# Kernel tuning notes

Measured on AMD Instinct MI355X. Metric: run time of the kernel, lower is better.

## Reference

```python
import jax, jax.numpy as jnp
import numpy as np

N = 100000
E = 3200000
H = 128
C = 40


def setup_inputs() -> dict:
    key = jax.random.key(0)
    ks = jax.random.split(key, 7)
    x = jax.random.normal(ks[0], (N, H), dtype=jnp.float32)
    edge_src = jax.random.randint(ks[1], (E,), 0, N, dtype=jnp.int32)
    edge_dst = jnp.sort(jax.random.randint(ks[2], (E,), 0, N, dtype=jnp.int32))
    edge_w = jax.random.uniform(ks[3], (E,), dtype=jnp.float32)
    s = 1.0 / np.sqrt(H)
    W0 = jax.random.normal(ks[4], (H, H), dtype=jnp.float32) * s
    W1 = jax.random.normal(ks[5], (H, H), dtype=jnp.float32) * s
    W2 = jax.random.normal(ks[6], (H, C), dtype=jnp.float32) * s
    return {"x": x, "edge_src": edge_src, "edge_dst": edge_dst,
            "edge_w": edge_w, "W0": W0, "W1": W1, "W2": W2}


def _spmm(h, edge_src, edge_dst, edge_w):
    # out[i] = sum_{e: dst_e == i} w_e * h[src_e]   (sparse adj @ h)
    msgs = h[edge_src] * edge_w[:, None]          # [E, d]
    return jax.ops.segment_sum(msgs, edge_dst, num_segments=N)


def reference(x, edge_src, edge_dst, edge_w, W0, W1, W2):
    # layer 1: tanh(Linear(spmm(adj, x)))  (dropout is identity in eval mode)
    h = jnp.tanh(_spmm(x, edge_src, edge_dst, edge_w) @ W0)
    # layer 2
    h = jnp.tanh(_spmm(h, edge_src, edge_dst, edge_w) @ W1)
    # output layer (GraphConvSparse default activation is tanh here too)
    out = jnp.tanh(_spmm(h, edge_src, edge_dst, edge_w) @ W2)
    return out
```

## Files before the change

kernel.cpp:

```cpp
#include <hip/hip_runtime.h>
#include <hip/hip_fp16.h>

#define NN 100000
#define NPAD 100096
#define EE 3200000
#define HH 128
#define CC 40

typedef _Float16 f16x8 __attribute__((ext_vector_type(8)));
typedef float f32x4 __attribute__((ext_vector_type(4)));

__global__ void build_rp(const int* __restrict__ dst, int* __restrict__ rp) {
    int i = blockIdx.x * blockDim.x + threadIdx.x;
    if (i > NN) return;
    int lo = 0, hi = EE;
    while (lo < hi) {
        int mid = (lo + hi) >> 1;
        if (dst[mid] < i) lo = mid + 1; else hi = mid;
    }
    rp[i] = lo;
}

__global__ __launch_bounds__(256) void f32_to_f16(const float* __restrict__ in,
                                                  __half* __restrict__ out, int n) {
    int base = (blockIdx.x * 256 + threadIdx.x) * 8;
    if (base >= n) return;
    float4 a = *(const float4*)(in + base);
    float4 b = *(const float4*)(in + base + 4);
    __half2 h[4];
    h[0] = __floats2half2_rn(a.x, a.y);
    h[1] = __floats2half2_rn(a.z, a.w);
    h[2] = __floats2half2_rn(b.x, b.y);
    h[3] = __floats2half2_rn(b.z, b.w);
    *(float4*)(out + base) = *(float4*)h;
}

__global__ __launch_bounds__(256) void prep_edges(const int* __restrict__ src,
                                                  const float* __restrict__ w,
                                                  int4* __restrict__ ew) {
    int i = blockIdx.x * 256 + threadIdx.x;
    if (i >= EE / 4) return;
    int4 s = ((const int4*)src)[i];
    float4 f = ((const float4*)w)[i];
    int4 a, b;
    a.x = s.x; a.y = __float_as_int(f.x); a.z = s.y; a.w = __float_as_int(f.y);
    b.x = s.z; b.y = __float_as_int(f.z); b.z = s.w; b.w = __float_as_int(f.w);
    ew[2 * i] = a; ew[2 * i + 1] = b;
}

__global__ __launch_bounds__(256) void prep_weights(const float* __restrict__ W0,
                                                    const float* __restrict__ W1,
                                                    const float* __restrict__ W2,
                                                    __half* __restrict__ W0t,
                                                    __half* __restrict__ W1t,
                                                    __half* __restrict__ W2t) {
    int i = blockIdx.x * 256 + threadIdx.x;
    if (i < HH * HH) {
        int c = i >> 7, k = i & 127;
        W0t[i] = __float2half_rn(W0[k * HH + c]);
        W1t[i] = __float2half_rn(W1[k * HH + c]);
    }
    if (i < 64 * HH) {
        int c = i >> 7, k = i & 127;
        W2t[i] = __float2half_rn(c < CC ? W2[k * CC + c] : 0.f);
    }
}

__global__ __launch_bounds__(256) void spmm_h16(const __half* __restrict__ h,
                                                const int2* __restrict__ ew,
                                                const int* __restrict__ rp,
                                                __half* __restrict__ out) {
    int node = blockIdx.x * 4 + (threadIdx.x >> 6);
    int l = threadIdx.x & 63;
    if (node >= NN) return;
    int e0 = __builtin_amdgcn_readfirstlane(rp[node]);
    int e1 = __builtin_amdgcn_readfirstlane(rp[node + 1]);
    int g = l >> 4, r = l & 15;
    const f16x8* __restrict__ hrow = (const f16x8*)h;
    float acc[8] = {};
    int e = e0;
    if ((e & 1) && e < e1) {
        int2 pr = ew[e];
        float wk = (g == 0) ? __int_as_float(pr.y) : 0.f;
        f16x8 v = hrow[(size_t)pr.x * 16 + r];
#pragma unroll
        for (int j = 0; j < 8; ++j) acc[j] = fmaf(wk, (float)v[j], acc[j]);
        ++e;
    }
    int efull = e + ((e1 - e) & ~15);
    for (; e < efull; e += 16) {
        const int4* pp = (const int4*)(ew + e + 4 * g);
        int4 pa = pp[0];
        int4 pb = pp[1];
        f16x8 v0 = hrow[(size_t)pa.x * 16 + r];
        f16x8 v1 = hrow[(size_t)pa.z * 16 + r];
        f16x8 v2 = hrow[(size_t)pb.x * 16 + r];
        f16x8 v3 = hrow[(size_t)pb.z * 16 + r];
        float w0 = __int_as_float(pa.y), w1 = __int_as_float(pa.w);
        float w2 = __int_as_float(pb.y), w3 = __int_as_float(pb.w);
#pragma unroll
        for (int j = 0; j < 8; ++j) acc[j] = fmaf(w0, (float)v0[j], acc[j]);
#pragma unroll
        for (int j = 0; j < 8; ++j) acc[j] = fmaf(w1, (float)v1[j], acc[j]);
#pragma unroll
        for (int j = 0; j < 8; ++j) acc[j] = fmaf(w2, (float)v2[j], acc[j]);
#pragma unroll
        for (int j = 0; j < 8; ++j) acc[j] = fmaf(w3, (float)v3[j], acc[j]);
    }
    if (e < e1) {
#pragma unroll
        for (int k = 0; k < 4; ++k) {
            int idx = e + 4 * g + k;
            bool val = idx < e1;
            int2 pr = ew[val ? idx : e0];
            float wk = val ? __int_as_float(pr.y) : 0.f;
            f16x8 v = hrow[(size_t)pr.x * 16 + r];
#pragma unroll
            for (int j = 0; j < 8; ++j) acc[j] = fmaf(wk, (float)v[j], acc[j]);
        }
    }
#pragma unroll
    for (int j = 0; j < 8; ++j) {
        acc[j] += __shfl_xor(acc[j], 16);
        acc[j] += __shfl_xor(acc[j], 32);
    }
    if (l < 16) {
        __half2 hv[4];
#pragma unroll
        for (int j = 0; j < 4; ++j) hv[j] = __floats2half2_rn(acc[2 * j], acc[2 * j + 1]);
        *(float4*)(out + (size_t)node * HH + r * 8) = *(float4*)hv;
    }
}

__global__ __launch_bounds__(256) void spmm40_tanh(const __half* __restrict__ gpad,
                                                   const int2* __restrict__ ew,
                                                   const int* __restrict__ rp,
                                                   float* __restrict__ out) {
    int node = blockIdx.x * 4 + (threadIdx.x >> 6);
    int l = threadIdx.x & 63;
    if (node >= NN) return;
    int e0 = __builtin_amdgcn_readfirstlane(rp[node]);
    int e1 = __builtin_amdgcn_readfirstlane(rp[node + 1]);
    int g = l >> 3, r = l & 7;
    const f16x8* __restrict__ grow = (const f16x8*)gpad;
    float acc[8] = {};
    int e = e0;
    if ((e & 1) && e < e1) {
        int2 pr = ew[e];
        float wk = (g == 0) ? __int_as_float(pr.y) : 0.f;
        f16x8 v = grow[(size_t)pr.x * 8 + r];
#pragma unroll
        for (int j = 0; j < 8; ++j) acc[j] = fmaf(wk, (float)v[j], acc[j]);
        ++e;
    }
    int efull = e + ((e1 - e) & ~15);
    for (; e < efull; e += 16) {
        int4 pa = *(const int4*)(ew + e + 2 * g);
        f16x8 v0 = grow[(size_t)pa.x * 8 + r];
        f16x8 v1 = grow[(size_t)pa.z * 8 + r];
        float w0 = __int_as_float(pa.y), w1 = __int_as_float(pa.w);
#pragma unroll
        for (int j = 0; j < 8; ++j) acc[j] = fmaf(w0, (float)v0[j], acc[j]);
#pragma unroll
        for (int j = 0; j < 8; ++j) acc[j] = fmaf(w1, (float)v1[j], acc[j]);
    }
    if (e < e1) {
#pragma unroll
        for (int k = 0; k < 2; ++k) {
            int idx = e + 2 * g + k;
            bool val = idx < e1;
            int2 pr = ew[val ? idx : e0];
            float wk = val ? __int_as_float(pr.y) : 0.f;
            f16x8 v = grow[(size_t)pr.x * 8 + r];
#pragma unroll
            for (int j = 0; j < 8; ++j) acc[j] = fmaf(wk, (float)v[j], acc[j]);
        }
    }
#pragma unroll
    for (int j = 0; j < 8; ++j) {
        acc[j] += __shfl_xor(acc[j], 8);
        acc[j] += __shfl_xor(acc[j], 16);
        acc[j] += __shfl_xor(acc[j], 32);
    }
    if (l < 5) {
        float o[8];
#pragma unroll
        for (int j = 0; j < 8; ++j) o[j] = tanhf(acc[j]);
        *(float4*)(out + (size_t)node * CC + r * 8) = *(float4*)&o[0];
        *(float4*)(out + (size_t)node * CC + r * 8 + 4) = *(float4*)&o[4];
    }
}

__global__ __launch_bounds__(256) void gemm_mfma_tanh(const __half* __restrict__ A,
                                                      const __half* __restrict__ Wt,
                                                      __half* __restrict__ out) {
    int wave = threadIdx.x >> 6, l = threadIdx.x & 63;
    int r0 = blockIdx.x * 64 + wave * 16;
    int lr = l & 15, lg = l >> 4;
    const _Float16* Af = (const _Float16*)A;
    const _Float16* Wf = (const _Float16*)Wt;
    int arow = r0 + lr;
    f16x8 a[4];
#pragma unroll
    for (int kb = 0; kb < 4; ++kb)
        a[kb] = *(const f16x8*)(Af + (size_t)arow * HH + kb * 32 + lg * 8);
#pragma unroll
    for (int ct = 0; ct < 8; ++ct) {
        f32x4 acc = {0.f, 0.f, 0.f, 0.f};
#pragma unroll
        for (int kb = 0; kb < 4; ++kb) {
            f16x8 b = *(const f16x8*)(Wf + (size_t)(ct * 16 + lr) * HH + kb * 32 + lg * 8);
            acc = __builtin_amdgcn_mfma_f32_16x16x32_f16(a[kb], b, acc, 0, 0, 0);
        }
#pragma unroll
        for (int r = 0; r < 4; ++r) {
            int row = r0 + lg * 4 + r;
            if (row < NN)
                out[(size_t)row * HH + ct * 16 + lr] = __float2half_rn(tanhf(acc[r]));
        }
    }
}

__global__ __launch_bounds__(256) void gemm40_mfma(const __half* __restrict__ A,
                                                   const __half* __restrict__ Wt,
                                                   __half* __restrict__ out) {
    int wave = threadIdx.x >> 6, l = threadIdx.x & 63;
    int r0 = blockIdx.x * 64 + wave * 16;
    int lr = l & 15, lg = l >> 4;
    const _Float16* Af = (const _Float16*)A;
    const _Float16* Wf = (const _Float16*)Wt;
    int arow = r0 + lr;
    f16x8 a[4];
#pragma unroll
    for (int kb = 0; kb < 4; ++kb)
        a[kb] = *(const f16x8*)(Af + (size_t)arow * HH + kb * 32 + lg * 8);
#pragma unroll
    for (int ct = 0; ct < 4; ++ct) {
        f32x4 acc = {0.f, 0.f, 0.f, 0.f};
#pragma unroll
        for (int kb = 0; kb < 4; ++kb) {
            f16x8 b = *(const f16x8*)(Wf + (size_t)(ct * 16 + lr) * HH + kb * 32 + lg * 8);
            acc = __builtin_amdgcn_mfma_f32_16x16x32_f16(a[kb], b, acc, 0, 0, 0);
        }
        int col = ct * 16 + lr;
#pragma unroll
        for (int r = 0; r < 4; ++r) {
            int row = r0 + lg * 4 + r;
            if (row < NN)
                out[(size_t)row * 64 + col] = __float2half_rn(acc[r]);
        }
    }
}

extern "C" void kernel_launch(void* const* d_in, const int* in_sizes, int n_in,
                              void* d_out, int out_size, void* d_ws, size_t ws_size,
                              hipStream_t stream) {
    const float* x    = (const float*)d_in[0];
    const int*   esrc = (const int*)d_in[1];
    const int*   edst = (const int*)d_in[2];
    const float* ew_f = (const float*)d_in[3];
    const float* W0   = (const float*)d_in[4];
    const float* W1   = (const float*)d_in[5];
    const float* W2   = (const float*)d_in[6];
    float* out = (float*)d_out;

    char* ws = (char*)d_ws;
    size_t off = 0;
    int* rp = (int*)(ws + off);          off += (((size_t)(NN + 1) * 4) + 511) & ~(size_t)511;
    __half* buf0 = (__half*)(ws + off);  off += (size_t)NPAD * HH * sizeof(__half);
    __half* sA = (__half*)(ws + off);    off += (size_t)NPAD * HH * sizeof(__half);
    __half* hb = (__half*)(ws + off);    off += (size_t)NPAD * HH * sizeof(__half);
    int2* ew = (int2*)(ws + off);        off += (size_t)EE * sizeof(int2);
    __half* W0t = (__half*)(ws + off);   off += (size_t)HH * HH * sizeof(__half);
    __half* W1t = (__half*)(ws + off);   off += (size_t)HH * HH * sizeof(__half);
    __half* W2t = (__half*)(ws + off);   off += (size_t)64 * HH * sizeof(__half);
    __half* xh = buf0;
    __half* gb = buf0;

    build_rp<<<(NN + 256) / 256, 256, 0, stream>>>(edst, rp);
    f32_to_f16<<<(NN * HH) / (256 * 8), 256, 0, stream>>>(x, xh, NN * HH);
    prep_edges<<<(EE / 4 + 255) / 256, 256, 0, stream>>>(esrc, ew_f, (int4*)ew);
    prep_weights<<<64, 256, 0, stream>>>(W0, W1, W2, W0t, W1t, W2t);

    int gemm_grid = NPAD / 64;
    spmm_h16<<<NN / 4, 256, 0, stream>>>(xh, ew, rp, sA);
    gemm_mfma_tanh<<<gemm_grid, 256, 0, stream>>>(sA, W0t, hb);
    spmm_h16<<<NN / 4, 256, 0, stream>>>(hb, ew, rp, sA);
    gemm_mfma_tanh<<<gemm_grid, 256, 0, stream>>>(sA, W1t, hb);
    gemm40_mfma<<<gemm_grid, 256, 0, stream>>>(hb, W2t, gb);
    spmm40_tanh<<<NN / 4, 256, 0, stream>>>(gb, ew, rp, out);
}
```

Baseline: 514.6 us.

## Fuse prep kernels and layer-2 GEMMs, stage GEMM output via LDS, fast tanh

Merges the three preprocessing kernels into one launch. Fuses the W1 GEMM+tanh with the W2 GEMM so the layer-2 hidden state goes through LDS instead of a global round-trip. GEMM outputs are staged in shared memory so global stores are 16-byte vector writes rather than scattered 2-byte ones. tanhf is replaced by an exp/rcp approximation, which trades a little accuracy for fewer instructions.

```diff
diff --git a/kernel.cpp b/kernel.cpp
--- a/kernel.cpp
+++ b/kernel.cpp
@@ -9,6 +9,11 @@
 
 typedef _Float16 f16x8 __attribute__((ext_vector_type(8)));
 typedef float f32x4 __attribute__((ext_vector_type(4)));
+
+__device__ __forceinline__ float fast_tanh(float x) {
+    float t = __expf(2.f * fminf(x, 15.f));
+    return (t - 1.f) * __builtin_amdgcn_rcpf(t + 1.f);
+}
 
 __global__ void build_rp(const int* __restrict__ dst, int* __restrict__ rp) {
     int i = blockIdx.x * blockDim.x + threadIdx.x;
@@ -21,48 +26,47 @@
     rp[i] = lo;
 }
 
-__global__ __launch_bounds__(256) void f32_to_f16(const float* __restrict__ in,
-                                                  __half* __restrict__ out, int n) {
-    int base = (blockIdx.x * 256 + threadIdx.x) * 8;
-    if (base >= n) return;
-    float4 a = *(const float4*)(in + base);
-    float4 b = *(const float4*)(in + base + 4);
-    __half2 h[4];
-    h[0] = __floats2half2_rn(a.x, a.y);
-    h[1] = __floats2half2_rn(a.z, a.w);
-    h[2] = __floats2half2_rn(b.x, b.y);
-    h[3] = __floats2half2_rn(b.z, b.w);
-    *(float4*)(out + base) = *(float4*)h;
-}
-
-__global__ __launch_bounds__(256) void prep_edges(const int* __restrict__ src,
-                                                  const float* __restrict__ w,
-                                                  int4* __restrict__ ew) {
-    int i = blockIdx.x * 256 + threadIdx.x;
-    if (i >= EE / 4) return;
-    int4 s = ((const int4*)src)[i];
-    float4 f = ((const float4*)w)[i];
-    int4 a, b;
-    a.x = s.x; a.y = __float_as_int(f.x); a.z = s.y; a.w = __float_as_int(f.y);
-    b.x = s.z; b.y = __float_as_int(f.z); b.z = s.w; b.w = __float_as_int(f.w);
-    ew[2 * i] = a; ew[2 * i + 1] = b;
-}
-
-__global__ __launch_bounds__(256) void prep_weights(const float* __restrict__ W0,
-                                                    const float* __restrict__ W1,
-                                                    const float* __restrict__ W2,
-                                                    __half* __restrict__ W0t,
-                                                    __half* __restrict__ W1t,
-                                                    __half* __restrict__ W2t) {
-    int i = blockIdx.x * 256 + threadIdx.x;
-    if (i < HH * HH) {
-        int c = i >> 7, k = i & 127;
-        W0t[i] = __float2half_rn(W0[k * HH + c]);
-        W1t[i] = __float2half_rn(W1[k * HH + c]);
-    }
-    if (i < 64 * HH) {
-        int c = i >> 7, k = i & 127;
-        W2t[i] = __float2half_rn(c < CC ? W2[k * CC + c] : 0.f);
+__global__ __launch_bounds__(256) void prep_all(const float* __restrict__ x,
+                                                const int* __restrict__ src,
+                                                const float* __restrict__ w,
+                                                const float* __restrict__ W0,
+                                                const float* __restrict__ W1,
+                                                const float* __restrict__ W2,
+                                                __half* __restrict__ xh,
+                                                int4* __restrict__ ew,
+                                                __half* __restrict__ W0t,
+                                                __half* __restrict__ W1t,
+                                                __half* __restrict__ W2t) {
+    int b = blockIdx.x, tid = threadIdx.x;
+    if (b < 6250) {
+        int base = (b * 256 + tid) * 8;
+        float4 a = *(const float4*)(x + base);
+        float4 c = *(const float4*)(x + base + 4);
+        __half2 h[4];
+        h[0] = __floats2half2_rn(a.x, a.y);
+        h[1] = __floats2half2_rn(a.z, a.w);
+        h[2] = __floats2half2_rn(c.x, c.y);
+        h[3] = __floats2half2_rn(c.z, c.w);
+        *(float4*)(xh + base) = *(float4*)h;
+    } else if (b < 9375) {
+        int i = (b - 6250) * 256 + tid;
+        int4 s = ((const int4*)src)[i];
+        float4 f = ((const float4*)w)[i];
+        int4 pa, pb;
+        pa.x = s.x; pa.y = __float_as_int(f.x); pa.z = s.y; pa.w = __float_as_int(f.y);
+        pb.x = s.z; pb.y = __float_as_int(f.z); pb.z = s.w; pb.w = __float_as_int(f.w);
+        ew[2 * i] = pa; ew[2 * i + 1] = pb;
+    } else {
+        int i = (b - 9375) * 256 + tid;
+        if (i < HH * HH) {
+            int c = i >> 7, k = i & 127;
+            W0t[i] = __float2half_rn(W0[k * HH + c]);
+            W1t[i] = __float2half_rn(W1[k * HH + c]);
+        }
+        if (i < 64 * HH) {
+            int c = i >> 7, k = i & 127;
+            W2t[i] = __float2half_rn(c < CC ? W2[k * CC + c] : 0.f);
+        }
     }
 }
 
@@ -185,25 +189,25 @@
     if (l < 5) {
         float o[8];
 #pragma unroll
-        for (int j = 0; j < 8; ++j) o[j] = tanhf(acc[j]);
+        for (int j = 0; j < 8; ++j) o[j] = fast_tanh(acc[j]);
         *(float4*)(out + (size_t)node * CC + r * 8) = *(float4*)&o[0];
         *(float4*)(out + (size_t)node * CC + r * 8 + 4) = *(float4*)&o[4];
     }
 }
 
-__global__ __launch_bounds__(256) void gemm_mfma_tanh(const __half* __restrict__ A,
+__global__ __launch_bounds__(256) void gemm_tanh_mfma(const __half* __restrict__ A,
                                                       const __half* __restrict__ Wt,
                                                       __half* __restrict__ out) {
+    __shared__ _Float16 st[4][16][136];
     int wave = threadIdx.x >> 6, l = threadIdx.x & 63;
     int r0 = blockIdx.x * 64 + wave * 16;
     int lr = l & 15, lg = l >> 4;
     const _Float16* Af = (const _Float16*)A;
     const _Float16* Wf = (const _Float16*)Wt;
-    int arow = r0 + lr;
     f16x8 a[4];
 #pragma unroll
     for (int kb = 0; kb < 4; ++kb)
-        a[kb] = *(const f16x8*)(Af + (size_t)arow * HH + kb * 32 + lg * 8);
+        a[kb] = *(const f16x8*)(Af + (size_t)(r0 + lr) * HH + kb * 32 + lg * 8);
 #pragma unroll
     for (int ct = 0; ct < 8; ++ct) {
         f32x4 acc = {0.f, 0.f, 0.f, 0.f};
@@ -213,42 +217,69 @@
             acc = __builtin_amdgcn_mfma_f32_16x16x32_f16(a[kb], b, acc, 0, 0, 0);
         }
 #pragma unroll
-        for (int r = 0; r < 4; ++r) {
-            int row = r0 + lg * 4 + r;
-            if (row < NN)
-                out[(size_t)row * HH + ct * 16 + lr] = __float2half_rn(tanhf(acc[r]));
-        }
-    }
-}
-
-__global__ __launch_bounds__(256) void gemm40_mfma(const __half* __restrict__ A,
-                                                   const __half* __restrict__ Wt,
-                                                   __half* __restrict__ out) {
+        for (int r = 0; r < 4; ++r)
+            st[wave][lg * 4 + r][ct * 16 + lr] = (_Float16)fast_tanh(acc[r]);
+    }
+#pragma unroll
+    for (int i = 0; i < 4; ++i) {
+        int row = lg + 4 * i;
+        int grow = r0 + row;
+        f16x8 v = *(const f16x8*)&st[wave][row][lr * 8];
+        if (grow < NN)
+            *(f16x8*)((_Float16*)out + (size_t)grow * HH + lr * 8) = v;
+    }
+}
+
+__global__ __launch_bounds__(256) void gemm2_fused(const __half* __restrict__ A,
+                                                   const __half* __restrict__ W1t,
+                                                   const __half* __restrict__ W2t,
+                                                   __half* __restrict__ gout) {
+    __shared__ _Float16 st[4][16][136];
     int wave = threadIdx.x >> 6, l = threadIdx.x & 63;
     int r0 = blockIdx.x * 64 + wave * 16;
     int lr = l & 15, lg = l >> 4;
     const _Float16* Af = (const _Float16*)A;
-    const _Float16* Wf = (const _Float16*)Wt;
-    int arow = r0 + lr;
+    const _Float16* W1f = (const _Float16*)W1t;
+    const _Float16* W2f = (const _Float16*)W2t;
     f16x8 a[4];
 #pragma unroll
     for (int kb = 0; kb < 4; ++kb)
-        a[kb] = *(const f16x8*)(Af + (size_t)arow * HH + kb * 32 + lg * 8);
+        a[kb] = *(const f16x8*)(Af + (size_t)(r0 + lr) * HH + kb * 32 + lg * 8);
+#pragma unroll
+    for (int ct = 0; ct < 8; ++ct) {
+        f32x4 acc = {0.f, 0.f, 0.f, 0.f};
+#pragma unroll
+        for (int kb = 0; kb < 4; ++kb) {
+            f16x8 b = *(const f16x8*)(W1f + (size_t)(ct * 16 + lr) * HH + kb * 32 + lg * 8);
+            acc = __builtin_amdgcn_mfma_f32_16x16x32_f16(a[kb], b, acc, 0, 0, 0);
+        }
+#pragma unroll
+        for (int r = 0; r < 4; ++r)
+            st[wave][lg * 4 + r][ct * 16 + lr] = (_Float16)fast_tanh(acc[r]);
+    }
+    f16x8 a2[4];
+#pragma unroll
+    for (int kb = 0; kb < 4; ++kb)
+        a2[kb] = *(const f16x8*)&st[wave][lr][kb * 32 + lg * 8];
 #pragma unroll
     for (int ct = 0; ct < 4; ++ct) {
         f32x4 acc = {0.f, 0.f, 0.f, 0.f};
 #pragma unroll
         for (int kb = 0; kb < 4; ++kb) {
-            f16x8 b = *(const f16x8*)(Wf + (size_t)(ct * 16 + lr) * HH + kb * 32 + lg * 8);
-            acc = __builtin_amdgcn_mfma_f32_16x16x32_f16(a[kb], b, acc, 0, 0, 0);
-        }
-        int col = ct * 16 + lr;
-#pragma unroll
-        for (int r = 0; r < 4; ++r) {
-            int row = r0 + lg * 4 + r;
-            if (row < NN)
-                out[(size_t)row * 64 + col] = __float2half_rn(acc[r]);
-        }
+            f16x8 b = *(const f16x8*)(W2f + (size_t)(ct * 16 + lr) * HH + kb * 32 + lg * 8);
+            acc = __builtin_amdgcn_mfma_f32_16x16x32_f16(a2[kb], b, acc, 0, 0, 0);
+        }
+#pragma unroll
+        for (int r = 0; r < 4; ++r)
+            st[wave][lg * 4 + r][ct * 16 + lr] = (_Float16)acc[r];
+    }
+#pragma unroll
+    for (int i = 0; i < 2; ++i) {
+        int row = (l >> 3) + 8 * i;
+        int grow = r0 + row;
+        f16x8 v = *(const f16x8*)&st[wave][row][(l & 7) * 8];
+        if (grow < NN)
+            *(f16x8*)((_Float16*)gout + (size_t)grow * 64 + (l & 7) * 8) = v;
     }
 }
 
@@ -278,15 +309,13 @@
     __half* gb = buf0;
 
     build_rp<<<(NN + 256) / 256, 256, 0, stream>>>(edst, rp);
-    f32_to_f16<<<(NN * HH) / (256 * 8), 256, 0, stream>>>(x, xh, NN * HH);
-    prep_edges<<<(EE / 4 + 255) / 256, 256, 0, stream>>>(esrc, ew_f, (int4*)ew);
-    prep_weights<<<64, 256, 0, stream>>>(W0, W1, W2, W0t, W1t, W2t);
+    prep_all<<<9439, 256, 0, stream>>>(x, esrc, ew_f, W0, W1, W2,
+                                       xh, (int4*)ew, W0t, W1t, W2t);
 
     int gemm_grid = NPAD / 64;
     spmm_h16<<<NN / 4, 256, 0, stream>>>(xh, ew, rp, sA);
-    gemm_mfma_tanh<<<gemm_grid, 256, 0, stream>>>(sA, W0t, hb);
+    gemm_tanh_mfma<<<gemm_grid, 256, 0, stream>>>(sA, W0t, hb);
     spmm_h16<<<NN / 4, 256, 0, stream>>>(hb, ew, rp, sA);
-    gemm_mfma_tanh<<<gemm_grid, 256, 0, stream>>>(sA, W1t, hb);
-    gemm40_mfma<<<gemm_grid, 256, 0, stream>>>(hb, W2t, gb);
+    gemm2_fused<<<gemm_grid, 256, 0, stream>>>(sA, W1t, W2t, gb);
     spmm40_tanh<<<NN / 4, 256, 0, stream>>>(gb, ew, rp, out);
 }
```

After: 483.2 us. -6.1%, faster.
